# Optimization experiments

Measured on AMD Instinct MI355X. Metric: run time of the kernel, lower is better.

The kernel has to match this reference:

```python
import jax, jax.numpy as jnp
import numpy as np

B = 256          # batch size
D = 512          # feature_size
P = 5            # num_parts
NC = 11003       # num_classes
SEGC = 6         # segmentation classes
H = 64           # mask spatial size
SCALE = 28.0
ALPHA, BETA = 0.6, 0.4
SP, SN = 10.0, 40.0
TOPK = 8


def _l2n(x, axis):
    return x / jnp.linalg.norm(x, axis=axis, keepdims=True)


def setup_inputs() -> dict:
    key = jax.random.key(0)
    ks = jax.random.split(key, 10)
    return {
        "visual_embed": jax.random.normal(ks[0], (B, D), jnp.float32),
        "textual_embed": jax.random.normal(ks[1], (B, D), jnp.float32),
        "part_embed": jax.random.normal(ks[2], (P, B, D), jnp.float32),
        "attribute_embed": jax.random.normal(ks[3], (P, B, D), jnp.float32),
        "seg_feat": jax.random.normal(ks[4], (B * P, SEGC, H, H), jnp.float32),
        "W": jax.random.normal(ks[5], (D, NC), jnp.float32),
        "labels": jax.random.randint(ks[6], (B,), 0, NC, jnp.int64) if jax.config.jax_enable_x64 else jax.random.randint(ks[6], (B,), 0, NC, jnp.int32),
        "masks": jax.random.randint(ks[7], (B * P, H, H), 0, SEGC, jnp.int32),
        "vmask": jax.random.randint(ks[8], (B, P), 0, 2).astype(bool),
        "tmask": jax.random.randint(ks[9], (B, P), 0, 2).astype(bool),
    }


def _instance_loss(visual_embed, textual_embed, W, labels):
    vn = _l2n(visual_embed, 1)
    tn = _l2n(textual_embed, 1)
    Wn = _l2n(W, 0)
    v_logits = SCALE * (vn @ Wn)          # [B, NC]
    t_logits = SCALE * (tn @ Wn)
    idx = jnp.arange(labels.shape[0])
    v_loss = -jax.nn.log_softmax(v_logits, axis=-1)[idx, labels].mean()
    t_loss = -jax.nn.log_softmax(t_logits, axis=-1)[idx, labels].mean()
    return v_loss + t_loss


def _mask_loss(seg_feat, masks):
    logp = jax.nn.log_softmax(seg_feat, axis=1)                      # [BP, C, H, H]
    ce = -jnp.take_along_axis(logp, masks[:, None, :, :], axis=1)[:, 0]
    return P * ce.mean()


def _global_align_loss(visual_embed, textual_embed, labels):
    vn = _l2n(visual_embed, 1)
    tn = _l2n(textual_embed, 1)
    sim = vn @ tn.T                                                  # [B, B]
    match = labels[:, None] == labels[None, :]
    Lp = jax.nn.softplus(-SP * (sim - ALPHA))
    Ln = jax.nn.softplus(SN * (sim - BETA))
    # original loops over rows then columns, each covering the full matrix
    return 2.0 * jnp.where(match, Lp, Ln).sum() / labels.shape[0]


def _local_align_loss(part_embed, attribute_embed, labels, vmask, tmask):
    pe = _l2n(part_embed, 2)
    ae = _l2n(attribute_embed, 2)
    match = labels[:, None] == labels[None, :]
    bsz = labels.shape[0]
    total = jnp.float32(0.0)
    for i in range(P):  # small fixed loop over parts
        pm = vmask[:, i]
        am = tmask[:, i]
        sim = pe[i] @ ae[i].T                                        # [B, B]
        r1 = jnp.argsort(-sim, axis=1)
        r2 = jnp.argsort(-sim.T, axis=1)
        # NOTE: original code indexes rank1/rank2 with the PART index i
        # (not the sample index j), so the pseudo-label boost is constant
        # across samples within a part; reproduced faithfully.
        fwd1 = r1[i, :TOPK]
        hit1 = (r2[fwd1, :TOPK] == i).any(axis=1)
        boost1 = jnp.zeros(bsz, bool).at[fwd1].set(hit1)
        fwd2 = r2[i, :TOPK]
        hit2 = (r1[fwd2, :TOPK] == i).any(axis=1)
        boost2 = jnp.zeros(bsz, bool).at[fwd2].set(hit2)
        Lp = jax.nn.softplus(-SP * (sim - ALPHA))
        Ln = jax.nn.softplus(SN * (sim - BETA))
        # branch 1: rows j with pm[j], columns k with am[k]
        pos1 = match | boost1[None, :]
        w1 = (pm[:, None] & am[None, :]).astype(sim.dtype)
        b1 = (jnp.where(pos1, Lp, Ln) * w1).sum()
        # branch 2: samples j with pm[j]&am[j], rows k with pm[k]; pred = sim[k, j]
        pos2 = match | boost2[None, :]
        w2 = ((pm & am)[:, None] & pm[None, :]).astype(sim.dtype)
        b2 = (jnp.where(pos2, Lp.T, Ln.T) * w2).sum()
        total = total + (b1 + b2) / bsz
    return total / P


def reference(visual_embed, textual_embed, part_embed, attribute_embed, seg_feat, W,
              labels, masks, vmask, tmask):
    instance_loss = _instance_loss(visual_embed, textual_embed, W, labels)
    mask_loss = _mask_loss(seg_feat, masks)
    global_align_loss = _global_align_loss(visual_embed, textual_embed, labels)
    local_align_loss = _local_align_loss(part_embed, attribute_embed, labels, vmask, tmask)
    return (instance_loss, mask_loss, global_align_loss, local_align_loss)
```

## Files before the change

kernel.cpp:

```cpp
#include <hip/hip_runtime.h>
#include <stdint.h>
#include <stddef.h>

#define BB 256
#define DD 512
#define PP 5
#define NCLS 11003
#define NCP 11008
#define SEGC 6
#define SCALEF 28.0f
#define ALPHAF 0.6f
#define BETAF 0.4f
#define SPF 10.0f
#define SNF 40.0f

typedef __attribute__((ext_vector_type(8))) short bf16x8;
typedef __attribute__((ext_vector_type(4))) float f32x4;

__device__ __forceinline__ float waveSum(float v) {
#pragma unroll
    for (int o = 32; o; o >>= 1) v += __shfl_down(v, o);
    return v;
}

__device__ __forceinline__ float softplusf(float x) {
    return fmaxf(x, 0.f) + log1pf(__expf(-fabsf(x)));
}

__device__ __forceinline__ short to_bf16(float f) {
    uint32_t u = __float_as_uint(f);
    uint32_t r = (u + 0x7FFFu + ((u >> 16) & 1u)) >> 16;
    return (short)r;
}

__global__ __launch_bounds__(256) void convert_k(const void* labels_raw,
                                                 const void* vm_raw,
                                                 const void* tm_raw,
                                                 int* __restrict__ labs,
                                                 unsigned char* __restrict__ vmb,
                                                 unsigned char* __restrict__ tmb) {
    __shared__ int is64, v32, t32;
    if (threadIdx.x == 0) {
        const int* L = (const int*)labels_raw;
        int f = 1;
        for (int j = 0; j < 16; j++) if (L[2 * j + 1] != 0) f = 0;
        is64 = f;
        const int* V = (const int*)vm_raw;
        f = 1;
        for (int j = 0; j < 16; j++) if ((unsigned)V[j] > 1u) f = 0;
        v32 = f;
        const int* T = (const int*)tm_raw;
        f = 1;
        for (int j = 0; j < 16; j++) if ((unsigned)T[j] > 1u) f = 0;
        t32 = f;
    }
    __syncthreads();
    int i = threadIdx.x;
    if (i < BB) {
        if (is64) labs[i] = (int)((const long long*)labels_raw)[i];
        else      labs[i] = ((const int*)labels_raw)[i];
    }
    for (int j = i; j < BB * PP; j += 256) {
        vmb[j] = v32 ? (unsigned char)(((const int*)vm_raw)[j] != 0)
                     : (unsigned char)(((const unsigned char*)vm_raw)[j] != 0);
        tmb[j] = t32 ? (unsigned char)(((const int*)tm_raw)[j] != 0)
                     : (unsigned char)(((const unsigned char*)tm_raw)[j] != 0);
    }
}

__global__ __launch_bounds__(256) void norm_rows_k(const float* __restrict__ src,
                                                   float* __restrict__ dst,
                                                   short* __restrict__ Xp,
                                                   int row_base) {
    int row = blockIdx.x;
    const float* s = src + (size_t)row * DD;
    float v0 = s[threadIdx.x];
    float v1 = s[threadIdx.x + 256];
    float ss = v0 * v0 + v1 * v1;
    __shared__ float red[4];
    __shared__ float inv;
    float v = waveSum(ss);
    if ((threadIdx.x & 63) == 0) red[threadIdx.x >> 6] = v;
    __syncthreads();
    if (threadIdx.x == 0) inv = 1.0f / sqrtf(red[0] + red[1] + red[2] + red[3]);
    __syncthreads();
    float a = v0 * inv, b = v1 * inv;
    float* d = dst + (size_t)row * DD;
    d[threadIdx.x] = a;
    d[threadIdx.x + 256] = b;
    if (Xp) {
        int prow = row_base + row;
        int rt = prow >> 4, rl = prow & 15;
#pragma unroll
        for (int h = 0; h < 2; h++) {
            int c = threadIdx.x + h * 256;
            float val = h ? b : a;
            int kt = c >> 5;
            int lh = (c & 31) >> 3;
            int i = c & 7;
            int lane = (lh << 4) | rl;
            Xp[((size_t)(rt * 16 + kt) * 64 + lane) * 8 + i] = to_bf16(val);
        }
    }
}

__global__ __launch_bounds__(256) void wtrans_k(const float* __restrict__ W,
                                                short* __restrict__ Wp,
                                                float* __restrict__ swn_sq) {
    __shared__ short tile[32][66];
    __shared__ float colsum[64];
    int c0 = blockIdx.x * 64, k0 = blockIdx.y * 32;
    int t = threadIdx.x;
    if (t < 64) colsum[t] = 0.f;
    __syncthreads();
    int cl64 = t & 63, kl = t >> 6;
    float ss = 0.f;
#pragma unroll
    for (int it = 0; it < 8; it++) {
        int k = k0 + kl + it * 4;
        int c = c0 + cl64;
        float w = (c < NCLS) ? W[(size_t)k * NCLS + c] : 0.f;
        ss = fmaf(w, w, ss);
        tile[kl + it * 4][cl64] = to_bf16(w);
    }
    atomicAdd(&colsum[cl64], ss);
    __syncthreads();
    int ctl = t >> 6, lane = t & 63;
    int cl = lane & 15, lh = lane >> 4;
    bf16x8 v;
#pragma unroll
    for (int i = 0; i < 8; i++) v[i] = tile[lh * 8 + i][ctl * 16 + cl];
    int ct = blockIdx.x * 4 + ctl;
    *(bf16x8*)(Wp + ((size_t)(ct * 16 + blockIdx.y) * 64 + lane) * 8) = v;
    if (t < 64) atomicAdd(&swn_sq[c0 + t], colsum[t]);
}

__global__ __launch_bounds__(256) void logits_mfma_k(const short* __restrict__ Xp,
                                                     const short* __restrict__ Wp,
                                                     const float* __restrict__ swn_sq,
                                                     float* __restrict__ sumexp) {
    int wave = threadIdx.x >> 6;
    int lane = threadIdx.x & 63;
    int l15 = lane & 15, lh = lane >> 4;
    int rt = blockIdx.y * 4 + wave;
    int ct0 = blockIdx.x * 4;
    f32x4 acc0 = {0.f, 0.f, 0.f, 0.f};
    f32x4 acc1 = acc0, acc2 = acc0, acc3 = acc0;
    const short* ap = Xp + (size_t)rt * 16 * 64 * 8 + lane * 8;
    const short* bp = Wp + (size_t)ct0 * 16 * 64 * 8 + lane * 8;
#pragma unroll
    for (int kt = 0; kt < 16; kt++) {
        bf16x8 a  = *(const bf16x8*)(ap + (size_t)kt * 512);
        bf16x8 b0 = *(const bf16x8*)(bp + (size_t)kt * 512);
        bf16x8 b1 = *(const bf16x8*)(bp + (size_t)(16 * 512) + kt * 512);
        bf16x8 b2 = *(const bf16x8*)(bp + (size_t)(32 * 512) + kt * 512);
        bf16x8 b3 = *(const bf16x8*)(bp + (size_t)(48 * 512) + kt * 512);
        acc0 = __builtin_amdgcn_mfma_f32_16x16x32_bf16(a, b0, acc0, 0, 0, 0);
        acc1 = __builtin_amdgcn_mfma_f32_16x16x32_bf16(a, b1, acc1, 0, 0, 0);
        acc2 = __builtin_amdgcn_mfma_f32_16x16x32_bf16(a, b2, acc2, 0, 0, 0);
        acc3 = __builtin_amdgcn_mfma_f32_16x16x32_bf16(a, b3, acc3, 0, 0, 0);
    }
    float s0 = 0.f, s1 = 0.f, s2 = 0.f, s3 = 0.f;
#pragma unroll
    for (int j = 0; j < 4; j++) {
        int c = (ct0 + j) * 16 + l15;
        bool valid = c < NCLS;
        float sc = valid ? SCALEF / sqrtf(swn_sq[c]) : 0.f;
        f32x4 accj = (j == 0) ? acc0 : (j == 1) ? acc1 : (j == 2) ? acc2 : acc3;
        s0 += valid ? __expf(accj[0] * sc) : 0.f;
        s1 += valid ? __expf(accj[1] * sc) : 0.f;
        s2 += valid ? __expf(accj[2] * sc) : 0.f;
        s3 += valid ? __expf(accj[3] * sc) : 0.f;
    }
#pragma unroll
    for (int o = 1; o < 16; o <<= 1) {
        s0 += __shfl_xor(s0, o);
        s1 += __shfl_xor(s1, o);
        s2 += __shfl_xor(s2, o);
        s3 += __shfl_xor(s3, o);
    }
    if (l15 == 0) {
        int rbase = rt * 16 + 4 * lh;
        atomicAdd(&sumexp[rbase + 0], s0);
        atomicAdd(&sumexp[rbase + 1], s1);
        atomicAdd(&sumexp[rbase + 2], s2);
        atomicAdd(&sumexp[rbase + 3], s3);
    }
}

__global__ __launch_bounds__(256) void inst_label_k(const float* __restrict__ Xn,
                                                    const float* __restrict__ W,
                                                    const float* __restrict__ swn_sq,
                                                    const float* __restrict__ sumexp,
                                                    const int* __restrict__ labs,
                                                    double* __restrict__ iacc) {
    int i = blockIdx.x;
    int t = threadIdx.x;
    int lab = labs[i];
    float dv = 0.f, dt_ = 0.f;
    for (int k = t; k < DD; k += 256) {
        float w = W[(size_t)k * NCLS + lab];
        dv = fmaf(Xn[(size_t)i * DD + k], w, dv);
        dt_ = fmaf(Xn[(size_t)(BB + i) * DD + k], w, dt_);
    }
    __shared__ float rv[4], rt[4];
    float a = waveSum(dv), b = waveSum(dt_);
    if ((t & 63) == 0) { rv[t >> 6] = a; rt[t >> 6] = b; }
    __syncthreads();
    if (t == 0) {
        float sc = SCALEF / sqrtf(swn_sq[lab]);
        float dvs = (rv[0] + rv[1] + rv[2] + rv[3]) * sc;
        float dts = (rt[0] + rt[1] + rt[2] + rt[3]) * sc;
        float li = (logf(sumexp[i]) - dvs) + (logf(sumexp[BB + i]) - dts);
        atomicAdd(iacc, (double)li);
    }
}

__global__ __launch_bounds__(256) void mask_loss_k(const float* __restrict__ seg,
                                                   const int* __restrict__ masks,
                                                   double* __restrict__ acc) {
    int tid = blockIdx.x * 256 + threadIdx.x;
    int n = tid >> 10;
    int q = (tid & 1023) << 2;
    const float* p = seg + (size_t)n * (SEGC * 4096) + q;
    float4 x0 = *(const float4*)(p);
    float4 x1 = *(const float4*)(p + 4096);
    float4 x2 = *(const float4*)(p + 8192);
    float4 x3 = *(const float4*)(p + 12288);
    float4 x4 = *(const float4*)(p + 16384);
    float4 x5 = *(const float4*)(p + 20480);
    int4 mm = *(const int4*)(masks + (size_t)n * 4096 + q);
    float tot = 0.f;
#pragma unroll
    for (int j = 0; j < 4; j++) {
        float a0 = ((const float*)&x0)[j];
        float a1 = ((const float*)&x1)[j];
        float a2 = ((const float*)&x2)[j];
        float a3 = ((const float*)&x3)[j];
        float a4 = ((const float*)&x4)[j];
        float a5 = ((const float*)&x5)[j];
        int m = ((const int*)&mm)[j];
        float mx = fmaxf(fmaxf(fmaxf(a0, a1), fmaxf(a2, a3)), fmaxf(a4, a5));
        float se = __expf(a0 - mx) + __expf(a1 - mx) + __expf(a2 - mx) +
                   __expf(a3 - mx) + __expf(a4 - mx) + __expf(a5 - mx);
        float xm = (m == 0) ? a0 : (m == 1) ? a1 : (m == 2) ? a2
                 : (m == 3) ? a3 : (m == 4) ? a4 : a5;
        tot += logf(se) + mx - xm;
    }
    __shared__ float red[4];
    float v = waveSum(tot);
    if ((threadIdx.x & 63) == 0) red[threadIdx.x >> 6] = v;
    __syncthreads();
    if (threadIdx.x == 0)
        atomicAdd(&acc[blockIdx.x & 63], (double)(red[0] + red[1] + red[2] + red[3]));
}

__global__ __launch_bounds__(256) void sim_k(const float* __restrict__ vn,
                                             const float* __restrict__ tn,
                                             const float* __restrict__ pn,
                                             const float* __restrict__ an,
                                             float* __restrict__ sims) {
    int z = blockIdx.z;
    const float* X;
    const float* Y;
    if (z == 0) { X = vn; Y = tn; }
    else { X = pn + (size_t)(z - 1) * BB * DD; Y = an + (size_t)(z - 1) * BB * DD; }
    float* C = sims + (size_t)z * BB * BB;
    int row0 = blockIdx.y * 32, col0 = blockIdx.x * 32;
    int tx = threadIdx.x & 15, ty = threadIdx.x >> 4;
    __shared__ float Xs[32][33], Ys[32][33];
    float a00 = 0, a01 = 0, a10 = 0, a11 = 0;
    for (int kc = 0; kc < DD; kc += 32) {
#pragma unroll
        for (int l = 0; l < 4; l++) {
            int idx = threadIdx.x + l * 256;
            int r = idx >> 5, kk = idx & 31;
            Xs[r][kk] = X[(size_t)(row0 + r) * DD + kc + kk];
            Ys[r][kk] = Y[(size_t)(col0 + r) * DD + kc + kk];
        }
        __syncthreads();
#pragma unroll
        for (int kk = 0; kk < 32; kk++) {
            float x0 = Xs[ty * 2][kk], x1 = Xs[ty * 2 + 1][kk];
            float y0 = Ys[tx * 2][kk], y1 = Ys[tx * 2 + 1][kk];
            a00 = fmaf(x0, y0, a00);
            a01 = fmaf(x0, y1, a01);
            a10 = fmaf(x1, y0, a10);
            a11 = fmaf(x1, y1, a11);
        }
        __syncthreads();
    }
    int r = row0 + ty * 2, c = col0 + tx * 2;
    C[(size_t)r * BB + c] = a00;
    C[(size_t)r * BB + c + 1] = a01;
    C[(size_t)(r + 1) * BB + c] = a10;
    C[(size_t)(r + 1) * BB + c + 1] = a11;
}

__global__ __launch_bounds__(256) void boost_k(const float* __restrict__ sims,
                                               unsigned char* __restrict__ b1,
                                               unsigned char* __restrict__ b2) {
    int i = blockIdx.x;
    const float* S = sims + (size_t)(i + 1) * BB * BB;
    int c = threadIdx.x;
    __shared__ float rowv[BB], colv[BB];
    rowv[c] = S[(size_t)i * BB + c];
    colv[c] = S[(size_t)c * BB + i];
    __syncthreads();
    float rv = rowv[c], cv = colv[c];
    int rank1 = 0, rank2 = 0;
    for (int j = 0; j < BB; j++) {
        rank1 += rowv[j] > rv;
        rank2 += colv[j] > cv;
    }
    unsigned char bo1 = 0, bo2 = 0;
    if (rank1 < 8) {
        int cnt = 0;
        for (int a = 0; a < BB; a++) cnt += S[(size_t)a * BB + c] > rv;
        bo1 = (cnt < 8);
    }
    if (rank2 < 8) {
        int cnt = 0;
        for (int b = 0; b < BB; b++) cnt += S[(size_t)c * BB + b] > cv;
        bo2 = (cnt < 8);
    }
    b1[i * BB + c] = bo1;
    b2[i * BB + c] = bo2;
}

__global__ __launch_bounds__(256) void lalign_k(const float* __restrict__ sims,
                                                const int* __restrict__ labs,
                                                const unsigned char* __restrict__ vmb,
                                                const unsigned char* __restrict__ tmb,
                                                const unsigned char* __restrict__ b1,
                                                const unsigned char* __restrict__ b2,
                                                double* __restrict__ accL,
                                                double* __restrict__ accG) {
    int i = blockIdx.y, r = blockIdx.x, c = threadIdx.x;
    float v = 0.f;
    if (i == PP) {
        float s = sims[(size_t)r * BB + c];
        float x = (labs[r] == labs[c]) ? (-SPF * (s - ALPHAF)) : (SNF * (s - BETAF));
        v = softplusf(x);
    } else {
        const float* S = sims + (size_t)(i + 1) * BB * BB;
        float s = S[(size_t)r * BB + c];
        bool m = labs[r] == labs[c];
        float Lp = softplusf(-SPF * (s - ALPHAF));
        float Ln = softplusf(SNF * (s - BETAF));
        bool pmr = vmb[r * PP + i] != 0;
        bool pmc = vmb[c * PP + i] != 0;
        bool amc = tmb[c * PP + i] != 0;
        if (pmr && amc) v += (m || (b1[i * BB + c] != 0)) ? Lp : Ln;
        if (pmc && amc && pmr) v += (m || (b2[i * BB + r] != 0)) ? Lp : Ln;
    }
    __shared__ float red[4];
    v = waveSum(v);
    if ((threadIdx.x & 63) == 0) red[threadIdx.x >> 6] = v;
    __syncthreads();
    if (threadIdx.x == 0) {
        double* dst = (i == PP) ? &accG[r & 7] : &accL[r & 7];
        atomicAdd(dst, (double)(red[0] + red[1] + red[2] + red[3]));
    }
}

__global__ void finalize_k(const double* __restrict__ accs, float* __restrict__ out) {
    int t = threadIdx.x;
    double mv = accs[t];
    double gv = (t < 8) ? accs[64 + t] : 0.0;
    double lv = (t < 8) ? accs[72 + t] : 0.0;
#pragma unroll
    for (int o = 32; o; o >>= 1) {
        mv += __shfl_down(mv, o);
        gv += __shfl_down(gv, o);
        lv += __shfl_down(lv, o);
    }
    if (t == 0) {
        out[0] = (float)(accs[80] / (double)BB);
        out[1] = (float)((double)PP * mv / 5242880.0);
        out[2] = (float)(2.0 * gv / (double)BB);
        out[3] = (float)(lv / (double)(BB * PP));
    }
}

extern "C" void kernel_launch(void* const* d_in, const int* in_sizes, int n_in,
                              void* d_out, int out_size, void* d_ws, size_t ws_size,
                              hipStream_t stream) {
    const float* visual  = (const float*)d_in[0];
    const float* textual = (const float*)d_in[1];
    const float* part    = (const float*)d_in[2];
    const float* attr    = (const float*)d_in[3];
    const float* seg     = (const float*)d_in[4];
    const float* W       = (const float*)d_in[5];
    const void*  labels  = d_in[6];
    const int*   masks   = (const int*)d_in[7];
    const void*  vmask   = d_in[8];
    const void*  tmask   = d_in[9];
    float* out = (float*)d_out;

    float* ws = (float*)d_ws;
    short* Wp   = (short*)ws;
    float* base = ws + (size_t)NCP * DD / 2;
    short* Xp   = (short*)base;
    float* vn   = base + (size_t)BB * DD;
    float* tn   = vn + (size_t)BB * DD;
    float* pn   = tn + (size_t)BB * DD;
    float* an   = pn + (size_t)PP * BB * DD;
    float* swn_sq = an + (size_t)PP * BB * DD;
    float* sims = swn_sq + NCP;
    float* sumexp = sims + 6 * BB * BB;
    int* labs = (int*)(sumexp + 2 * BB);
    unsigned char* vmb = (unsigned char*)(labs + BB);
    unsigned char* tmb = vmb + BB * PP;
    unsigned char* b1  = tmb + BB * PP;
    unsigned char* b2  = b1 + BB * PP;
    uintptr_t aaddr = ((uintptr_t)(b2 + BB * PP) + 15) & ~(uintptr_t)15;
    double* accs = (double*)aaddr;

    hipMemsetAsync(sumexp, 0, 2 * BB * sizeof(float), stream);
    hipMemsetAsync(swn_sq, 0, NCP * sizeof(float), stream);
    hipMemsetAsync(accs, 0, 81 * sizeof(double), stream);

    convert_k<<<1, 256, 0, stream>>>(labels, vmask, tmask, labs, vmb, tmb);

    norm_rows_k<<<BB, 256, 0, stream>>>(visual, vn, Xp, 0);
    norm_rows_k<<<BB, 256, 0, stream>>>(textual, tn, Xp, BB);
    norm_rows_k<<<PP * BB, 256, 0, stream>>>(part, pn, nullptr, 0);
    norm_rows_k<<<PP * BB, 256, 0, stream>>>(attr, an, nullptr, 0);

    dim3 tg(NCP / 64, 16);
    wtrans_k<<<tg, 256, 0, stream>>>(W, Wp, swn_sq);

    dim3 mg(NCP / 64, 8);
    logits_mfma_k<<<mg, 256, 0, stream>>>(Xp, Wp, swn_sq, sumexp);
    inst_label_k<<<BB, 256, 0, stream>>>(vn, W, swn_sq, sumexp, labs, accs + 80);

    mask_loss_k<<<1310720 / 256, 256, 0, stream>>>(seg, masks, accs);

    dim3 sg(8, 8, 6);
    sim_k<<<sg, 256, 0, stream>>>(vn, tn, pn, an, sims);
    boost_k<<<PP, 256, 0, stream>>>(sims, b1, b2);

    dim3 lg(BB, PP + 1);
    lalign_k<<<lg, 256, 0, stream>>>(sims, labs, vmb, tmb, b1, b2, accs + 72, accs + 64);

    finalize_k<<<1, 64, 0, stream>>>(accs, out);
}
```

Before: 373.2 us.

## Merge independent kernels into three block-range-dispatched launches

Measured after the change: 343.1 us. 1.09x faster.

```diff
diff --git a/kernel.cpp b/kernel.cpp
--- a/kernel.cpp
+++ b/kernel.cpp
@@ -33,299 +33,317 @@
     return (short)r;
 }
 
-__global__ __launch_bounds__(256) void convert_k(const void* labels_raw,
-                                                 const void* vm_raw,
-                                                 const void* tm_raw,
-                                                 int* __restrict__ labs,
-                                                 unsigned char* __restrict__ vmb,
-                                                 unsigned char* __restrict__ tmb) {
-    __shared__ int is64, v32, t32;
-    if (threadIdx.x == 0) {
-        const int* L = (const int*)labels_raw;
-        int f = 1;
-        for (int j = 0; j < 16; j++) if (L[2 * j + 1] != 0) f = 0;
-        is64 = f;
-        const int* V = (const int*)vm_raw;
-        f = 1;
-        for (int j = 0; j < 16; j++) if ((unsigned)V[j] > 1u) f = 0;
-        v32 = f;
-        const int* T = (const int*)tm_raw;
-        f = 1;
-        for (int j = 0; j < 16; j++) if ((unsigned)T[j] > 1u) f = 0;
-        t32 = f;
-    }
-    __syncthreads();
-    int i = threadIdx.x;
-    if (i < BB) {
-        if (is64) labs[i] = (int)((const long long*)labels_raw)[i];
-        else      labs[i] = ((const int*)labels_raw)[i];
-    }
-    for (int j = i; j < BB * PP; j += 256) {
-        vmb[j] = v32 ? (unsigned char)(((const int*)vm_raw)[j] != 0)
-                     : (unsigned char)(((const unsigned char*)vm_raw)[j] != 0);
-        tmb[j] = t32 ? (unsigned char)(((const int*)tm_raw)[j] != 0)
-                     : (unsigned char)(((const unsigned char*)tm_raw)[j] != 0);
-    }
-}
-
-__global__ __launch_bounds__(256) void norm_rows_k(const float* __restrict__ src,
-                                                   float* __restrict__ dst,
-                                                   short* __restrict__ Xp,
-                                                   int row_base) {
-    int row = blockIdx.x;
-    const float* s = src + (size_t)row * DD;
-    float v0 = s[threadIdx.x];
-    float v1 = s[threadIdx.x + 256];
-    float ss = v0 * v0 + v1 * v1;
+__global__ __launch_bounds__(256) void prep_k(const float* __restrict__ vis,
+                                              const float* __restrict__ text,
+                                              const float* __restrict__ part,
+                                              const float* __restrict__ attr,
+                                              const float* __restrict__ W,
+                                              const void* labels_raw,
+                                              const void* vm_raw,
+                                              const void* tm_raw,
+                                              float* __restrict__ vn,
+                                              float* __restrict__ tn,
+                                              float* __restrict__ pn,
+                                              float* __restrict__ an,
+                                              short* __restrict__ Xp,
+                                              short* __restrict__ Wp,
+                                              float* __restrict__ swn_sq,
+                                              int* __restrict__ labs,
+                                              unsigned char* __restrict__ vmb,
+                                              unsigned char* __restrict__ tmb) {
+    __shared__ short tile[32][66];
+    __shared__ float colsum[64];
     __shared__ float red[4];
     __shared__ float inv;
-    float v = waveSum(ss);
-    if ((threadIdx.x & 63) == 0) red[threadIdx.x >> 6] = v;
-    __syncthreads();
-    if (threadIdx.x == 0) inv = 1.0f / sqrtf(red[0] + red[1] + red[2] + red[3]);
-    __syncthreads();
-    float a = v0 * inv, b = v1 * inv;
-    float* d = dst + (size_t)row * DD;
-    d[threadIdx.x] = a;
-    d[threadIdx.x + 256] = b;
-    if (Xp) {
-        int prow = row_base + row;
-        int rt = prow >> 4, rl = prow & 15;
-#pragma unroll
-        for (int h = 0; h < 2; h++) {
-            int c = threadIdx.x + h * 256;
-            float val = h ? b : a;
-            int kt = c >> 5;
-            int lh = (c & 31) >> 3;
-            int i = c & 7;
-            int lane = (lh << 4) | rl;
-            Xp[((size_t)(rt * 16 + kt) * 64 + lane) * 8 + i] = to_bf16(val);
-        }
-    }
-}
-
-__global__ __launch_bounds__(256) void wtrans_k(const float* __restrict__ W,
-                                                short* __restrict__ Wp,
-                                                float* __restrict__ swn_sq) {
-    __shared__ short tile[32][66];
-    __shared__ float colsum[64];
-    int c0 = blockIdx.x * 64, k0 = blockIdx.y * 32;
+    int bx = blockIdx.x;
     int t = threadIdx.x;
-    if (t < 64) colsum[t] = 0.f;
-    __syncthreads();
-    int cl64 = t & 63, kl = t >> 6;
-    float ss = 0.f;
-#pragma unroll
-    for (int it = 0; it < 8; it++) {
-        int k = k0 + kl + it * 4;
-        int c = c0 + cl64;
-        float w = (c < NCLS) ? W[(size_t)k * NCLS + c] : 0.f;
-        ss = fmaf(w, w, ss);
-        tile[kl + it * 4][cl64] = to_bf16(w);
-    }
-    atomicAdd(&colsum[cl64], ss);
-    __syncthreads();
-    int ctl = t >> 6, lane = t & 63;
-    int cl = lane & 15, lh = lane >> 4;
-    bf16x8 v;
-#pragma unroll
-    for (int i = 0; i < 8; i++) v[i] = tile[lh * 8 + i][ctl * 16 + cl];
-    int ct = blockIdx.x * 4 + ctl;
-    *(bf16x8*)(Wp + ((size_t)(ct * 16 + blockIdx.y) * 64 + lane) * 8) = v;
-    if (t < 64) atomicAdd(&swn_sq[c0 + t], colsum[t]);
-}
-
-__global__ __launch_bounds__(256) void logits_mfma_k(const short* __restrict__ Xp,
-                                                     const short* __restrict__ Wp,
-                                                     const float* __restrict__ swn_sq,
-                                                     float* __restrict__ sumexp) {
-    int wave = threadIdx.x >> 6;
-    int lane = threadIdx.x & 63;
-    int l15 = lane & 15, lh = lane >> 4;
-    int rt = blockIdx.y * 4 + wave;
-    int ct0 = blockIdx.x * 4;
-    f32x4 acc0 = {0.f, 0.f, 0.f, 0.f};
-    f32x4 acc1 = acc0, acc2 = acc0, acc3 = acc0;
-    const short* ap = Xp + (size_t)rt * 16 * 64 * 8 + lane * 8;
-    const short* bp = Wp + (size_t)ct0 * 16 * 64 * 8 + lane * 8;
-#pragma unroll
-    for (int kt = 0; kt < 16; kt++) {
-        bf16x8 a  = *(const bf16x8*)(ap + (size_t)kt * 512);
-        bf16x8 b0 = *(const bf16x8*)(bp + (size_t)kt * 512);
-        bf16x8 b1 = *(const bf16x8*)(bp + (size_t)(16 * 512) + kt * 512);
-        bf16x8 b2 = *(const bf16x8*)(bp + (size_t)(32 * 512) + kt * 512);
-        bf16x8 b3 = *(const bf16x8*)(bp + (size_t)(48 * 512) + kt * 512);
-        acc0 = __builtin_amdgcn_mfma_f32_16x16x32_bf16(a, b0, acc0, 0, 0, 0);
-        acc1 = __builtin_amdgcn_mfma_f32_16x16x32_bf16(a, b1, acc1, 0, 0, 0);
-        acc2 = __builtin_amdgcn_mfma_f32_16x16x32_bf16(a, b2, acc2, 0, 0, 0);
-        acc3 = __builtin_amdgcn_mfma_f32_16x16x32_bf16(a, b3, acc3, 0, 0, 0);
-    }
-    float s0 = 0.f, s1 = 0.f, s2 = 0.f, s3 = 0.f;
-#pragma unroll
-    for (int j = 0; j < 4; j++) {
-        int c = (ct0 + j) * 16 + l15;
-        bool valid = c < NCLS;
-        float sc = valid ? SCALEF / sqrtf(swn_sq[c]) : 0.f;
-        f32x4 accj = (j == 0) ? acc0 : (j == 1) ? acc1 : (j == 2) ? acc2 : acc3;
-        s0 += valid ? __expf(accj[0] * sc) : 0.f;
-        s1 += valid ? __expf(accj[1] * sc) : 0.f;
-        s2 += valid ? __expf(accj[2] * sc) : 0.f;
-        s3 += valid ? __expf(accj[3] * sc) : 0.f;
-    }
-#pragma unroll
-    for (int o = 1; o < 16; o <<= 1) {
-        s0 += __shfl_xor(s0, o);
-        s1 += __shfl_xor(s1, o);
-        s2 += __shfl_xor(s2, o);
-        s3 += __shfl_xor(s3, o);
-    }
-    if (l15 == 0) {
-        int rbase = rt * 16 + 4 * lh;
-        atomicAdd(&sumexp[rbase + 0], s0);
-        atomicAdd(&sumexp[rbase + 1], s1);
-        atomicAdd(&sumexp[rbase + 2], s2);
-        atomicAdd(&sumexp[rbase + 3], s3);
-    }
-}
-
-__global__ __launch_bounds__(256) void inst_label_k(const float* __restrict__ Xn,
-                                                    const float* __restrict__ W,
-                                                    const float* __restrict__ swn_sq,
-                                                    const float* __restrict__ sumexp,
-                                                    const int* __restrict__ labs,
-                                                    double* __restrict__ iacc) {
-    int i = blockIdx.x;
+    if (bx < 3072) {
+        const float* src;
+        float* dst;
+        short* Xpp = nullptr;
+        int row, row_base = 0;
+        if (bx < 256)       { src = vis;  dst = vn; Xpp = Xp; row = bx;        row_base = 0; }
+        else if (bx < 512)  { src = text; dst = tn; Xpp = Xp; row = bx - 256;  row_base = BB; }
+        else if (bx < 1792) { src = part; dst = pn; row = bx - 512; }
+        else                { src = attr; dst = an; row = bx - 1792; }
+        const float* s = src + (size_t)row * DD;
+        float v0 = s[t];
+        float v1 = s[t + 256];
+        float v = waveSum(v0 * v0 + v1 * v1);
+        if ((t & 63) == 0) red[t >> 6] = v;
+        __syncthreads();
+        if (t == 0) inv = 1.0f / sqrtf(red[0] + red[1] + red[2] + red[3]);
+        __syncthreads();
+        float a = v0 * inv, b = v1 * inv;
+        float* d = dst + (size_t)row * DD;
+        d[t] = a;
+        d[t + 256] = b;
+        if (Xpp) {
+            int prow = row_base + row;
+            int rt = prow >> 4, rl = prow & 15;
+#pragma unroll
+            for (int h = 0; h < 2; h++) {
+                int c = t + h * 256;
+                float val = h ? b : a;
+                int kt = c >> 5;
+                int lh = (c & 31) >> 3;
+                int i = c & 7;
+                int lane = (lh << 4) | rl;
+                Xpp[((size_t)(rt * 16 + kt) * 64 + lane) * 8 + i] = to_bf16(val);
+            }
+        }
+    } else if (bx < 5824) {
+        int idx = bx - 3072;
+        int bxw = idx % 172, byw = idx / 172;
+        int c0 = bxw * 64, k0 = byw * 32;
+        if (t < 64) colsum[t] = 0.f;
+        __syncthreads();
+        int cl64 = t & 63, kl = t >> 6;
+        float ss = 0.f;
+#pragma unroll
+        for (int it = 0; it < 8; it++) {
+            int k = k0 + kl + it * 4;
+            int c = c0 + cl64;
+            float w = (c < NCLS) ? W[(size_t)k * NCLS + c] : 0.f;
+            ss = fmaf(w, w, ss);
+            tile[kl + it * 4][cl64] = to_bf16(w);
+        }
+        atomicAdd(&colsum[cl64], ss);
+        __syncthreads();
+        int ctl = t >> 6, lane = t & 63;
+        int cl = lane & 15, lh = lane >> 4;
+        bf16x8 v;
+#pragma unroll
+        for (int i = 0; i < 8; i++) v[i] = tile[lh * 8 + i][ctl * 16 + cl];
+        int ct = bxw * 4 + ctl;
+        *(bf16x8*)(Wp + ((size_t)(ct * 16 + byw) * 64 + lane) * 8) = v;
+        if (t < 64) atomicAdd(&swn_sq[c0 + t], colsum[t]);
+    } else {
+        __shared__ int is64, v32, t32;
+        if (t == 0) {
+            const int* L = (const int*)labels_raw;
+            int f = 1;
+            for (int j = 0; j < 16; j++) if (L[2 * j + 1] != 0) f = 0;
+            is64 = f;
+            const int* V = (const int*)vm_raw;
+            f = 1;
+            for (int j = 0; j < 16; j++) if ((unsigned)V[j] > 1u) f = 0;
+            v32 = f;
+            const int* T = (const int*)tm_raw;
+            f = 1;
+            for (int j = 0; j < 16; j++) if ((unsigned)T[j] > 1u) f = 0;
+            t32 = f;
+        }
+        __syncthreads();
+        if (t < BB) {
+            if (is64) labs[t] = (int)((const long long*)labels_raw)[t];
+            else      labs[t] = ((const int*)labels_raw)[t];
+        }
+        for (int j = t; j < BB * PP; j += 256) {
+            vmb[j] = v32 ? (unsigned char)(((const int*)vm_raw)[j] != 0)
+                         : (unsigned char)(((const unsigned char*)vm_raw)[j] != 0);
+            tmb[j] = t32 ? (unsigned char)(((const int*)tm_raw)[j] != 0)
+                         : (unsigned char)(((const unsigned char*)tm_raw)[j] != 0);
+        }
+    }
+}
+
+__global__ __launch_bounds__(256) void heavy_k(const short* __restrict__ Xp,
+                                               const short* __restrict__ Wp,
+                                               const float* __restrict__ swn_sq,
+                                               float* __restrict__ sumexp,
+                                               const float* __restrict__ seg,
+                                               const int* __restrict__ masks,
+                                               double* __restrict__ macc,
+                                               const float* __restrict__ vn,
+                                               const float* __restrict__ tn,
+                                               const float* __restrict__ pn,
+                                               const float* __restrict__ an,
+                                               float* __restrict__ sims) {
+    __shared__ float Xs[32][33], Ys[32][33];
+    __shared__ float red[4];
+    int bx = blockIdx.x;
     int t = threadIdx.x;
-    int lab = labs[i];
-    float dv = 0.f, dt_ = 0.f;
-    for (int k = t; k < DD; k += 256) {
-        float w = W[(size_t)k * NCLS + lab];
-        dv = fmaf(Xn[(size_t)i * DD + k], w, dv);
-        dt_ = fmaf(Xn[(size_t)(BB + i) * DD + k], w, dt_);
-    }
-    __shared__ float rv[4], rt[4];
-    float a = waveSum(dv), b = waveSum(dt_);
-    if ((t & 63) == 0) { rv[t >> 6] = a; rt[t >> 6] = b; }
-    __syncthreads();
-    if (t == 0) {
-        float sc = SCALEF / sqrtf(swn_sq[lab]);
-        float dvs = (rv[0] + rv[1] + rv[2] + rv[3]) * sc;
-        float dts = (rt[0] + rt[1] + rt[2] + rt[3]) * sc;
-        float li = (logf(sumexp[i]) - dvs) + (logf(sumexp[BB + i]) - dts);
-        atomicAdd(iacc, (double)li);
-    }
-}
-
-__global__ __launch_bounds__(256) void mask_loss_k(const float* __restrict__ seg,
-                                                   const int* __restrict__ masks,
-                                                   double* __restrict__ acc) {
-    int tid = blockIdx.x * 256 + threadIdx.x;
-    int n = tid >> 10;
-    int q = (tid & 1023) << 2;
-    const float* p = seg + (size_t)n * (SEGC * 4096) + q;
-    float4 x0 = *(const float4*)(p);
-    float4 x1 = *(const float4*)(p + 4096);
-    float4 x2 = *(const float4*)(p + 8192);
-    float4 x3 = *(const float4*)(p + 12288);
-    float4 x4 = *(const float4*)(p + 16384);
-    float4 x5 = *(const float4*)(p + 20480);
-    int4 mm = *(const int4*)(masks + (size_t)n * 4096 + q);
-    float tot = 0.f;
-#pragma unroll
-    for (int j = 0; j < 4; j++) {
-        float a0 = ((const float*)&x0)[j];
-        float a1 = ((const float*)&x1)[j];
-        float a2 = ((const float*)&x2)[j];
-        float a3 = ((const float*)&x3)[j];
-        float a4 = ((const float*)&x4)[j];
-        float a5 = ((const float*)&x5)[j];
-        int m = ((const int*)&mm)[j];
-        float mx = fmaxf(fmaxf(fmaxf(a0, a1), fmaxf(a2, a3)), fmaxf(a4, a5));
-        float se = __expf(a0 - mx) + __expf(a1 - mx) + __expf(a2 - mx) +
-                   __expf(a3 - mx) + __expf(a4 - mx) + __expf(a5 - mx);
-        float xm = (m == 0) ? a0 : (m == 1) ? a1 : (m == 2) ? a2
-                 : (m == 3) ? a3 : (m == 4) ? a4 : a5;
-        tot += logf(se) + mx - xm;
-    }
-    __shared__ float red[4];
-    float v = waveSum(tot);
-    if ((threadIdx.x & 63) == 0) red[threadIdx.x >> 6] = v;
-    __syncthreads();
-    if (threadIdx.x == 0)
-        atomicAdd(&acc[blockIdx.x & 63], (double)(red[0] + red[1] + red[2] + red[3]));
-}
-
-__global__ __launch_bounds__(256) void sim_k(const float* __restrict__ vn,
-                                             const float* __restrict__ tn,
-                                             const float* __restrict__ pn,
-                                             const float* __restrict__ an,
-                                             float* __restrict__ sims) {
-    int z = blockIdx.z;
-    const float* X;
-    const float* Y;
-    if (z == 0) { X = vn; Y = tn; }
-    else { X = pn + (size_t)(z - 1) * BB * DD; Y = an + (size_t)(z - 1) * BB * DD; }
-    float* C = sims + (size_t)z * BB * BB;
-    int row0 = blockIdx.y * 32, col0 = blockIdx.x * 32;
-    int tx = threadIdx.x & 15, ty = threadIdx.x >> 4;
-    __shared__ float Xs[32][33], Ys[32][33];
-    float a00 = 0, a01 = 0, a10 = 0, a11 = 0;
-    for (int kc = 0; kc < DD; kc += 32) {
-#pragma unroll
-        for (int l = 0; l < 4; l++) {
-            int idx = threadIdx.x + l * 256;
-            int r = idx >> 5, kk = idx & 31;
-            Xs[r][kk] = X[(size_t)(row0 + r) * DD + kc + kk];
-            Ys[r][kk] = Y[(size_t)(col0 + r) * DD + kc + kk];
-        }
-        __syncthreads();
-#pragma unroll
-        for (int kk = 0; kk < 32; kk++) {
-            float x0 = Xs[ty * 2][kk], x1 = Xs[ty * 2 + 1][kk];
-            float y0 = Ys[tx * 2][kk], y1 = Ys[tx * 2 + 1][kk];
-            a00 = fmaf(x0, y0, a00);
-            a01 = fmaf(x0, y1, a01);
-            a10 = fmaf(x1, y0, a10);
-            a11 = fmaf(x1, y1, a11);
-        }
-        __syncthreads();
-    }
-    int r = row0 + ty * 2, c = col0 + tx * 2;
-    C[(size_t)r * BB + c] = a00;
-    C[(size_t)r * BB + c + 1] = a01;
-    C[(size_t)(r + 1) * BB + c] = a10;
-    C[(size_t)(r + 1) * BB + c + 1] = a11;
-}
-
-__global__ __launch_bounds__(256) void boost_k(const float* __restrict__ sims,
-                                               unsigned char* __restrict__ b1,
-                                               unsigned char* __restrict__ b2) {
-    int i = blockIdx.x;
-    const float* S = sims + (size_t)(i + 1) * BB * BB;
-    int c = threadIdx.x;
+    if (bx < 1376) {
+        int ctg = bx % 172, rtg = bx / 172;
+        int wave = t >> 6, lane = t & 63;
+        int l15 = lane & 15, lh = lane >> 4;
+        int rt = rtg * 4 + wave;
+        int ct0 = ctg * 4;
+        f32x4 acc0 = {0.f, 0.f, 0.f, 0.f};
+        f32x4 acc1 = acc0, acc2 = acc0, acc3 = acc0;
+        const short* ap = Xp + (size_t)rt * 16 * 64 * 8 + lane * 8;
+        const short* bp = Wp + (size_t)ct0 * 16 * 64 * 8 + lane * 8;
+#pragma unroll
+        for (int kt = 0; kt < 16; kt++) {
+            bf16x8 a  = *(const bf16x8*)(ap + (size_t)kt * 512);
+            bf16x8 b0 = *(const bf16x8*)(bp + (size_t)kt * 512);
+            bf16x8 b1 = *(const bf16x8*)(bp + (size_t)(16 * 512) + kt * 512);
+            bf16x8 b2 = *(const bf16x8*)(bp + (size_t)(32 * 512) + kt * 512);
+            bf16x8 b3 = *(const bf16x8*)(bp + (size_t)(48 * 512) + kt * 512);
+            acc0 = __builtin_amdgcn_mfma_f32_16x16x32_bf16(a, b0, acc0, 0, 0, 0);
+            acc1 = __builtin_amdgcn_mfma_f32_16x16x32_bf16(a, b1, acc1, 0, 0, 0);
+            acc2 = __builtin_amdgcn_mfma_f32_16x16x32_bf16(a, b2, acc2, 0, 0, 0);
+            acc3 = __builtin_amdgcn_mfma_f32_16x16x32_bf16(a, b3, acc3, 0, 0, 0);
+        }
+        float s0 = 0.f, s1 = 0.f, s2 = 0.f, s3 = 0.f;
+#pragma unroll
+        for (int j = 0; j < 4; j++) {
+            int c = (ct0 + j) * 16 + l15;
+            bool valid = c < NCLS;
+            float sc = valid ? SCALEF / sqrtf(swn_sq[c]) : 0.f;
+            f32x4 accj = (j == 0) ? acc0 : (j == 1) ? acc1 : (j == 2) ? acc2 : acc3;
+            s0 += valid ? __expf(accj[0] * sc) : 0.f;
+            s1 += valid ? __expf(accj[1] * sc) : 0.f;
+            s2 += valid ? __expf(accj[2] * sc) : 0.f;
+            s3 += valid ? __expf(accj[3] * sc) : 0.f;
+        }
+#pragma unroll
+        for (int o = 1; o < 16; o <<= 1) {
+            s0 += __shfl_xor(s0, o);
+            s1 += __shfl_xor(s1, o);
+            s2 += __shfl_xor(s2, o);
+            s3 += __shfl_xor(s3, o);
+        }
+        if (l15 == 0) {
+            int rbase = rt * 16 + 4 * lh;
+            atomicAdd(&sumexp[rbase + 0], s0);
+            atomicAdd(&sumexp[rbase + 1], s1);
+            atomicAdd(&sumexp[rbase + 2], s2);
+            atomicAdd(&sumexp[rbase + 3], s3);
+        }
+    } else if (bx < 6496) {
+        int tid = (bx - 1376) * 256 + t;
+        int n = tid >> 10;
+        int q = (tid & 1023) << 2;
+        const float* p = seg + (size_t)n * (SEGC * 4096) + q;
+        float4 x0 = *(const float4*)(p);
+        float4 x1 = *(const float4*)(p + 4096);
+        float4 x2 = *(const float4*)(p + 8192);
+        float4 x3 = *(const float4*)(p + 12288);
+        float4 x4 = *(const float4*)(p + 16384);
+        float4 x5 = *(const float4*)(p + 20480);
+        int4 mm = *(const int4*)(masks + (size_t)n * 4096 + q);
+        float tot = 0.f;
+#pragma unroll
+        for (int j = 0; j < 4; j++) {
+            float a0 = ((const float*)&x0)[j];
+            float a1 = ((const float*)&x1)[j];
+            float a2 = ((const float*)&x2)[j];
+            float a3 = ((const float*)&x3)[j];
+            float a4 = ((const float*)&x4)[j];
+            float a5 = ((const float*)&x5)[j];
+            int m = ((const int*)&mm)[j];
+            float mx = fmaxf(fmaxf(fmaxf(a0, a1), fmaxf(a2, a3)), fmaxf(a4, a5));
+            float se = __expf(a0 - mx) + __expf(a1 - mx) + __expf(a2 - mx) +
+                       __expf(a3 - mx) + __expf(a4 - mx) + __expf(a5 - mx);
+            float xm = (m == 0) ? a0 : (m == 1) ? a1 : (m == 2) ? a2
+                     : (m == 3) ? a3 : (m == 4) ? a4 : a5;
+            tot += logf(se) + mx - xm;
+        }
+        float v = waveSum(tot);
+        if ((t & 63) == 0) red[t >> 6] = v;
+        __syncthreads();
+        if (t == 0)
+            atomicAdd(&macc[bx & 63], (double)(red[0] + red[1] + red[2] + red[3]));
+    } else {
+        int idx2 = bx - 6496;
+        int z = idx2 >> 6;
+        int rem = idx2 & 63;
+        int col0 = (rem & 7) * 32, row0 = (rem >> 3) * 32;
+        const float* X;
+        const float* Y;
+        if (z == 0) { X = vn; Y = tn; }
+        else { X = pn + (size_t)(z - 1) * BB * DD; Y = an + (size_t)(z - 1) * BB * DD; }
+        float* C = sims + (size_t)z * BB * BB;
+        int tx = t & 15, ty = t >> 4;
+        float a00 = 0, a01 = 0, a10 = 0, a11 = 0;
+        for (int kc = 0; kc < DD; kc += 32) {
+#pragma unroll
+            for (int l = 0; l < 4; l++) {
+                int idx = t + l * 256;
+                int r = idx >> 5, kk = idx & 31;
+                Xs[r][kk] = X[(size_t)(row0 + r) * DD + kc + kk];
+                Ys[r][kk] = Y[(size_t)(col0 + r) * DD + kc + kk];
+            }
+            __syncthreads();
+#pragma unroll
+            for (int kk = 0; kk < 32; kk++) {
+                float x0 = Xs[ty * 2][kk], x1 = Xs[ty * 2 + 1][kk];
+                float y0 = Ys[tx * 2][kk], y1 = Ys[tx * 2 + 1][kk];
+                a00 = fmaf(x0, y0, a00);
+                a01 = fmaf(x0, y1, a01);
+                a10 = fmaf(x1, y0, a10);
+                a11 = fmaf(x1, y1, a11);
+            }
+            __syncthreads();
+        }
+        int r = row0 + ty * 2, c = col0 + tx * 2;
+        C[(size_t)r * BB + c] = a00;
+        C[(size_t)r * BB + c + 1] = a01;
+        C[(size_t)(r + 1) * BB + c] = a10;
+        C[(size_t)(r + 1) * BB + c + 1] = a11;
+    }
+}
+
+__global__ __launch_bounds__(256) void mid_k(const float* __restrict__ sims,
+                                             unsigned char* __restrict__ b1,
+                                             unsigned char* __restrict__ b2,
+                                             const float* __restrict__ Xn,
+                                             const float* __restrict__ W,
+                                             const float* __restrict__ swn_sq,
+                                             const float* __restrict__ sumexp,
+                                             const int* __restrict__ labs,
+                                             double* __restrict__ iacc) {
     __shared__ float rowv[BB], colv[BB];
-    rowv[c] = S[(size_t)i * BB + c];
-    colv[c] = S[(size_t)c * BB + i];
-    __syncthreads();
-    float rv = rowv[c], cv = colv[c];
-    int rank1 = 0, rank2 = 0;
-    for (int j = 0; j < BB; j++) {
-        rank1 += rowv[j] > rv;
-        rank2 += colv[j] > cv;
-    }
-    unsigned char bo1 = 0, bo2 = 0;
-    if (rank1 < 8) {
-        int cnt = 0;
-        for (int a = 0; a < BB; a++) cnt += S[(size_t)a * BB + c] > rv;
-        bo1 = (cnt < 8);
-    }
-    if (rank2 < 8) {
-        int cnt = 0;
-        for (int b = 0; b < BB; b++) cnt += S[(size_t)c * BB + b] > cv;
-        bo2 = (cnt < 8);
-    }
-    b1[i * BB + c] = bo1;
-    b2[i * BB + c] = bo2;
+    int bx = blockIdx.x;
+    int t = threadIdx.x;
+    if (bx < PP) {
+        int i = bx;
+        const float* S = sims + (size_t)(i + 1) * BB * BB;
+        int c = t;
+        rowv[c] = S[(size_t)i * BB + c];
+        colv[c] = S[(size_t)c * BB + i];
+        __syncthreads();
+        float rv = rowv[c], cv = colv[c];
+        int rank1 = 0, rank2 = 0;
+        for (int j = 0; j < BB; j++) {
+            rank1 += rowv[j] > rv;
+            rank2 += colv[j] > cv;
+        }
+        unsigned char bo1 = 0, bo2 = 0;
+        if (rank1 < 8) {
+            int cnt = 0;
+            for (int a = 0; a < BB; a++) cnt += S[(size_t)a * BB + c] > rv;
+            bo1 = (cnt < 8);
+        }
+        if (rank2 < 8) {
+            int cnt = 0;
+            for (int b = 0; b < BB; b++) cnt += S[(size_t)c * BB + b] > cv;
+            bo2 = (cnt < 8);
+        }
+        b1[i * BB + c] = bo1;
+        b2[i * BB + c] = bo2;
+    } else {
+        int i = bx - PP;
+        int lab = labs[i];
+        float dv = 0.f, dt_ = 0.f;
+        for (int k = t; k < DD; k += 256) {
+            float w = W[(size_t)k * NCLS + lab];
+            dv = fmaf(Xn[(size_t)i * DD + k], w, dv);
+            dt_ = fmaf(Xn[(size_t)(BB + i) * DD + k], w, dt_);
+        }
+        float a = waveSum(dv), b = waveSum(dt_);
+        if ((t & 63) == 0) { rowv[t >> 6] = a; colv[t >> 6] = b; }
+        __syncthreads();
+        if (t == 0) {
+            float sc = SCALEF / sqrtf(swn_sq[lab]);
+            float dvs = (rowv[0] + rowv[1] + rowv[2] + rowv[3]) * sc;
+            float dts = (colv[0] + colv[1] + colv[2] + colv[3]) * sc;
+            float li = (logf(sumexp[i]) - dvs) + (logf(sumexp[BB + i]) - dts);
+            atomicAdd(iacc, (double)li);
+        }
+    }
 }
 
 __global__ __launch_bounds__(256) void lalign_k(const float* __restrict__ sims,
@@ -421,25 +439,15 @@
     hipMemsetAsync(swn_sq, 0, NCP * sizeof(float), stream);
     hipMemsetAsync(accs, 0, 81 * sizeof(double), stream);
 
-    convert_k<<<1, 256, 0, stream>>>(labels, vmask, tmask, labs, vmb, tmb);
-
-    norm_rows_k<<<BB, 256, 0, stream>>>(visual, vn, Xp, 0);
-    norm_rows_k<<<BB, 256, 0, stream>>>(textual, tn, Xp, BB);
-    norm_rows_k<<<PP * BB, 256, 0, stream>>>(part, pn, nullptr, 0);
-    norm_rows_k<<<PP * BB, 256, 0, stream>>>(attr, an, nullptr, 0);
-
-    dim3 tg(NCP / 64, 16);
-    wtrans_k<<<tg, 256, 0, stream>>>(W, Wp, swn_sq);
-
-    dim3 mg(NCP / 64, 8);
-    logits_mfma_k<<<mg, 256, 0, stream>>>(Xp, Wp, swn_sq, sumexp);
-    inst_label_k<<<BB, 256, 0, stream>>>(vn, W, swn_sq, sumexp, labs, accs + 80);
-
-    mask_loss_k<<<1310720 / 256, 256, 0, stream>>>(seg, masks, accs);
-
-    dim3 sg(8, 8, 6);
-    sim_k<<<sg, 256, 0, stream>>>(vn, tn, pn, an, sims);
-    boost_k<<<PP, 256, 0, stream>>>(sims, b1, b2);
+    prep_k<<<5825, 256, 0, stream>>>(visual, textual, part, attr, W,
+                                     labels, vmask, tmask,
+                                     vn, tn, pn, an, Xp, Wp, swn_sq, labs, vmb, tmb);
+
+    heavy_k<<<6880, 256, 0, stream>>>(Xp, Wp, swn_sq, sumexp,
+                                      seg, masks, accs,
+                                      vn, tn, pn, an, sims);
+
+    mid_k<<<261, 256, 0, stream>>>(sims, b1, b2, vn, W, swn_sq, sumexp, labs, accs + 80);
 
     dim3 lg(BB, PP + 1);
     lalign_k<<<lg, 256, 0, stream>>>(sims, labs, vmb, tmb, b1, b2, accs + 72, accs + 64);
```
